# Kernel optimization log

Hardware: AMD Instinct MI355X
Metric: run time of the kernel (lower is better)

Reference implementation:

```python
import jax, jax.numpy as jnp
import numpy as np

BITS = 4
VALS_PER_WORD = 4  # four 4-bit nibbles packed per 16-bit word


def dequantize(w_packed, w_scale, w_bias, dtype):
    # w_packed: [out, groups, cols] int32, each word holds 4 nibbles (little-endian)
    out, g, cols = w_packed.shape
    shifts = jnp.arange(VALS_PER_WORD, dtype=jnp.int32) * BITS  # [4]
    # [out, groups, cols, 4] nibble values in [0, 15]
    q = (w_packed[..., None] >> shifts) & 0xF
    q = q.astype(dtype).reshape(out, g, cols * VALS_PER_WORD)
    w = q * w_scale + w_bias  # per-group affine dequant, scale/bias broadcast over group
    return w.reshape(out, g * cols * VALS_PER_WORD)  # [out, in]


def setup_inputs() -> dict:
    key = jax.random.key(0)
    k1, k2, k3, k4, k5 = jax.random.split(key, 5)
    B, S, IN, OUT, G = 2, 2048, 4096, 16384, 16
    cols = IN // G // VALS_PER_WORD  # 64 packed words per group
    return {
        "input": jax.random.normal(k1, (B, S, IN), dtype=jnp.float32),
        "w_packed": jax.random.randint(k2, (OUT, G, cols), 0, 65536, dtype=jnp.int32),
        "w_scale": jax.random.uniform(k3, (OUT, G, 1), dtype=jnp.float32) * 0.01,
        "w_bias": jax.random.normal(k4, (OUT, G, 1), dtype=jnp.float32) * 0.05,
        "bias": jax.random.normal(k5, (OUT,), dtype=jnp.float32),
    }


def reference(input, w_packed, w_scale, w_bias, bias):
    weight = dequantize(w_packed, w_scale, w_bias, input.dtype)  # [out, in]
    # F.linear: y = x @ W^T + b
    return jnp.einsum("bsi,oi->bso", input, weight) + bias
```

## Files before the change

### kernel.cpp

```cpp
#include <hip/hip_runtime.h>
#include <hip/hip_bf16.h>


typedef short bf16x8 __attribute__((ext_vector_type(8)));
typedef float f32x4 __attribute__((ext_vector_type(4)));
typedef int i32x4 __attribute__((ext_vector_type(4)));
typedef unsigned short u16;
typedef unsigned short u16x8 __attribute__((ext_vector_type(8)));

#define BM 128
#define BN 128
#define BK 64
#define THREADS 256

static __device__ __forceinline__ u16 f2bf(float f) {
    __hip_bfloat16 h = __float2bfloat16(f);
    return __builtin_bit_cast(u16, h);
}


__global__ void rowstat_kernel(const float* __restrict__ x, float* __restrict__ sx,
                               float* __restrict__ rsx, int K) {
    const int m = blockIdx.x;
    const int l = threadIdx.x;
    const float4* p = (const float4*)(x + (size_t)m * K);
    float mx = 0.f;
    for (int i = l; i < (K >> 2); i += 64) {
        const float4 v = p[i];
        mx = fmaxf(mx, fmaxf(fmaxf(fabsf(v.x), fabsf(v.y)),
                             fmaxf(fabsf(v.z), fabsf(v.w))));
    }
    #pragma unroll
    for (int o = 32; o; o >>= 1) mx = fmaxf(mx, __shfl_xor(mx, o));
    if (l == 0) {
        mx = fmaxf(mx, 1e-20f);
        sx[m]  = mx * (1.f / 127.f);
        rsx[m] = 127.f / mx;
    }
}

__global__ void quantX_kernel(const float* __restrict__ x, const float* __restrict__ rsx,
                              char* __restrict__ xq, int kshift, size_t n16) {
    size_t i = (size_t)blockIdx.x * blockDim.x + threadIdx.x;
    if (i >= n16) return;
    const int m = (int)((i * 16) >> kshift);
    const float r = rsx[m];
    const float4* px = (const float4*)(x + i * 16);
    int out[4];
    #pragma unroll
    for (int w = 0; w < 4; ++w) {
        const float4 v = px[w];
        const int b0 = __float2int_rn(v.x * r) & 0xFF;
        const int b1 = __float2int_rn(v.y * r) & 0xFF;
        const int b2 = __float2int_rn(v.z * r) & 0xFF;
        const int b3 = __float2int_rn(v.w * r) & 0xFF;
        out[w] = b0 | (b1 << 8) | (b2 << 16) | (b3 << 24);
    }
    *(int4*)(xq + i * 16) = make_int4(out[0], out[1], out[2], out[3]);
}

__global__ void rowscaleW_kernel(const float* __restrict__ Ws,
                                 const float* __restrict__ Wb,
                                 float* __restrict__ swr, float* __restrict__ rswr,
                                 int G, int N) {
    const int n = blockIdx.x * blockDim.x + threadIdx.x;
    if (n >= N) return;
    float mx = 1e-20f;
    for (int g = 0; g < G; ++g) {
        const float s = Ws[(size_t)n * G + g];
        const float b = Wb[(size_t)n * G + g];
        mx = fmaxf(mx, fmaxf(fabsf(b), fabsf(fmaf(15.f, s, b))));
    }
    swr[n]  = mx * (1.f / 127.f);
    rswr[n] = 127.f / mx;
}

__global__ void quantW_row_kernel(const int* __restrict__ Wp, const float* __restrict__ Ws,
                                  const float* __restrict__ Wb, const float* __restrict__ rswr,
                                  char* __restrict__ wq, int K, int G, int gshift,
                                  int kcshift, size_t nthr) {
    size_t t = (size_t)blockIdx.x * blockDim.x + threadIdx.x;
    if (t >= nthr) return;
    const int n  = (int)(t >> kcshift);
    const int kc = (int)(t & ((1u << kcshift) - 1));
    const int g  = (kc << 4) >> gshift;
    const float s = Ws[(size_t)n * G + g];
    const float b = Wb[(size_t)n * G + g];
    const float rs = rswr[n];
    const int4 wv = *(const int4*)(Wp + (size_t)n * (K >> 2) + ((size_t)kc << 2));
    const int wds[4] = {wv.x, wv.y, wv.z, wv.w};
    int out[4];
    #pragma unroll
    for (int w = 0; w < 4; ++w) {
        int o = 0;
        #pragma unroll
        for (int j = 0; j < 4; ++j) {
            const float v = fmaf((float)((wds[w] >> (4 * j)) & 0xF), s, b);
            o |= (__float2int_rn(v * rs) & 0xFF) << (8 * j);
        }
        out[w] = o;
    }
    *(int4*)(wq + t * 16) = make_int4(out[0], out[1], out[2], out[3]);
}


__global__ __launch_bounds__(256, 2)
void gql_gemm_i8t(const char* __restrict__ xq,
                  const char* __restrict__ wq,
                  const float* __restrict__ swr,
                  const float* __restrict__ sx,
                  const float* __restrict__ Bias,
                  float* __restrict__ Out,
                  int M, int N, int K)
{
    __shared__ __align__(16) char sA[2][256 * 64];
    __shared__ __align__(16) char sB[2][128 * 64];

    const int tid  = threadIdx.x;
    const int lane = tid & 63;
    const int wid  = tid >> 6;
    const int wm   = wid >> 1;
    const int wn   = wid & 1;

    const int nwg = gridDim.x;
    int wg = blockIdx.x;
    if ((nwg & 7) == 0) wg = (wg & 7) * (nwg >> 3) + (wg >> 3);
    const int nt = N / 128;
    const int m0 = (wg / nt) * 256;
    const int n0 = (wg % nt) * 128;

    const int fr = lane & 15;
    const int fq = lane >> 4;

    const int st_kc  = ((lane & 3) ^ ((lane >> 3) & 3)) << 4;
    const int st_rw  = lane >> 2;

    const int rq = (fq ^ ((fr >> 1) & 3)) << 4;

    i32x4 acc[8][4] = {};

    const int NT = K >> 6;

    auto stage = [&](int t, int buf) {
        const size_t k0 = (size_t)t << 6;
        #pragma unroll
        for (int i = 0; i < 4; ++i) {
            const int inst = wid + i * 4;
            const int row  = inst * 16 + st_rw;
            const char* src = xq + (size_t)(m0 + row) * K + k0 + st_kc;
            __builtin_amdgcn_global_load_lds(
                (const __attribute__((address_space(1))) void*)src,
                (__attribute__((address_space(3))) void*)&sA[buf][inst * 1024],
                16, 0, 0);
        }
        #pragma unroll
        for (int i = 0; i < 2; ++i) {
            const int inst = wid + i * 4;
            const int row  = inst * 16 + st_rw;
            const char* src = wq + (size_t)(n0 + row) * K + k0 + st_kc;
            __builtin_amdgcn_global_load_lds(
                (const __attribute__((address_space(1))) void*)src,
                (__attribute__((address_space(3))) void*)&sB[buf][inst * 1024],
                16, 0, 0);
        }
    };

    auto compute = [&](int buf) {
        i32x4 af[8], bfr[4];
        #pragma unroll
        for (int i = 0; i < 8; ++i) {
            const int row = wm * 128 + i * 16 + fr;
            const u16x8 raw = *(const u16x8*)(&sA[buf][row * 64 + rq]);
            af[i] = __builtin_bit_cast(i32x4, raw);
        }
        #pragma unroll
        for (int j = 0; j < 4; ++j) {
            const int row = wn * 64 + j * 16 + fr;
            const u16x8 raw = *(const u16x8*)(&sB[buf][row * 64 + rq]);
            bfr[j] = __builtin_bit_cast(i32x4, raw);
        }
        __builtin_amdgcn_s_setprio(1);
        #pragma unroll
        for (int i = 0; i < 8; ++i)
            #pragma unroll
            for (int j = 0; j < 4; ++j)
                acc[i][j] = __builtin_amdgcn_mfma_i32_16x16x64_i8(
                    af[i], bfr[j], acc[i][j], 0, 0, 0);
        __builtin_amdgcn_s_setprio(0);
    };

    stage(0, 0);
    int cur = 0;
    for (int t = 0; t < NT - 1; ++t) {
        stage(t + 1, cur ^ 1);
        __builtin_amdgcn_sched_barrier(0);
        asm volatile("s_waitcnt vmcnt(6)" ::: "memory");
        __builtin_amdgcn_s_barrier();
        asm volatile("" ::: "memory");
        compute(cur);
        __builtin_amdgcn_sched_barrier(0);
        asm volatile("" ::: "memory");
        __builtin_amdgcn_s_barrier();
        asm volatile("" ::: "memory");
        cur ^= 1;
    }
    asm volatile("s_waitcnt vmcnt(0)" ::: "memory");
    __builtin_amdgcn_s_barrier();
    asm volatile("" ::: "memory");
    compute(cur);

    #pragma unroll
    for (int j = 0; j < 4; ++j) {
        const int col = n0 + wn * 64 + j * 16 + fr;
        const float bv = Bias[col];
        const float sv = swr[col];
        #pragma unroll
        for (int i = 0; i < 8; ++i) {
            const int mb = m0 + wm * 128 + i * 16 + (fq << 2);
            #pragma unroll
            for (int r = 0; r < 4; ++r)
                Out[(size_t)(mb + r) * N + col] =
                    fmaf(sx[mb + r] * sv, (float)acc[i][j][r], bv);
        }
    }
}


__global__ void cvtA_kernel(const float* __restrict__ A, u16* __restrict__ wsA,
                            size_t n8) {
    size_t i = (size_t)blockIdx.x * blockDim.x + threadIdx.x;
    if (i >= n8) return;
    const float4 v0 = *(const float4*)(A + i * 8);
    const float4 v1 = *(const float4*)(A + i * 8 + 4);
    u16x8 h;
    h[0] = f2bf(v0.x); h[1] = f2bf(v0.y); h[2] = f2bf(v0.z); h[3] = f2bf(v0.w);
    h[4] = f2bf(v1.x); h[5] = f2bf(v1.y); h[6] = f2bf(v1.z); h[7] = f2bf(v1.w);
    *(u16x8*)(wsA + i * 8) = h;
}

__global__ void deqW_kernel(const int* __restrict__ Wp, const float* __restrict__ Ws,
                            const float* __restrict__ Wb, u16* __restrict__ wsW,
                            int K, int G, int gshift, int kgshift, size_t n8) {
    size_t t = (size_t)blockIdx.x * blockDim.x + threadIdx.x;
    if (t >= n8) return;
    const int n  = (int)(t >> kgshift);
    const int kg = (int)(t & ((1u << kgshift) - 1));
    const int k  = kg << 3;
    const int g  = k >> gshift;
    const float s = Ws[n * G + g];
    const float b = Wb[n * G + g];
    const int2 w2 = *(const int2*)(Wp + (size_t)n * (K >> 2) + (k >> 2));
    u16x8 h;
    #pragma unroll
    for (int j = 0; j < 4; ++j)
        h[j]     = f2bf(fmaf((float)((w2.x >> (4 * j)) & 0xF), s, b));
    #pragma unroll
    for (int j = 0; j < 4; ++j)
        h[4 + j] = f2bf(fmaf((float)((w2.y >> (4 * j)) & 0xF), s, b));
    *(u16x8*)(wsW + ((size_t)n << (kgshift + 3)) + k) = h;
}

__global__ __launch_bounds__(THREADS, 2)
void gql_gemm_pre(const u16* __restrict__ wsA,
                  const u16* __restrict__ wsW,
                  const float* __restrict__ Bias,
                  float* __restrict__ Out,
                  int M, int N, int K)
{
    __shared__ __align__(16) u16 sA[BM * BK];
    __shared__ __align__(16) u16 sB[BN * BK];

    const int tid  = threadIdx.x;
    const int lane = tid & 63;
    const int wid  = tid >> 6;

    const int nwg = gridDim.x;
    int wg = blockIdx.x;
    if ((nwg & 7) == 0) wg = (wg & 7) * (nwg >> 3) + (wg >> 3);
    const int nt     = N / BN;
    const int m0 = (wg / nt) * BM;
    const int n0 = (wg % nt) * BN;

    const int st_r  = (lane >> 3);
    const int st_g  = lane & 7;

    const int wr = (wid >> 1) << 6;
    const int wc = (wid & 1) << 6;
    const int fr = lane & 15;
    const int fq = lane >> 4;

    f32x4 acc[4][4] = {};

    for (int k0 = 0; k0 < K; k0 += BK) {
        __syncthreads();

        #pragma unroll
        for (int i = 0; i < 4; ++i) {
            const int r = wid * 32 + i * 8 + st_r;
            const int gsrc = (st_g ^ (r & 7)) << 3;
            const u16* srcA = wsA + (size_t)(m0 + r) * K + k0 + gsrc;
            const u16* srcB = wsW + (size_t)(n0 + r) * K + k0 + gsrc;
            __builtin_amdgcn_global_load_lds(
                (const __attribute__((address_space(1))) void*)srcA,
                (__attribute__((address_space(3))) void*)&sA[(wid * 32 + i * 8) * BK],
                16, 0, 0);
            __builtin_amdgcn_global_load_lds(
                (const __attribute__((address_space(1))) void*)srcB,
                (__attribute__((address_space(3))) void*)&sB[(wid * 32 + i * 8) * BK],
                16, 0, 0);
        }

        __syncthreads();

        #pragma unroll
        for (int sub = 0; sub < 2; ++sub) {
            const int kch = (sub << 2) + fq;
            bf16x8 af[4], bfg[4];
            #pragma unroll
            for (int i = 0; i < 4; ++i) {
                const int row = wr + i * 16 + fr;
                af[i] = *(const bf16x8*)((const char*)sA + row * (BK * 2)
                                         + (((kch ^ (row & 7)) << 4)));
            }
            #pragma unroll
            for (int j = 0; j < 4; ++j) {
                const int row = wc + j * 16 + fr;
                bfg[j] = *(const bf16x8*)((const char*)sB + row * (BK * 2)
                                          + (((kch ^ (row & 7)) << 4)));
            }
            #pragma unroll
            for (int i = 0; i < 4; ++i)
                #pragma unroll
                for (int j = 0; j < 4; ++j)
                    acc[i][j] = __builtin_amdgcn_mfma_f32_16x16x32_bf16(
                        af[i], bfg[j], acc[i][j], 0, 0, 0);
        }
    }

    #pragma unroll
    for (int j = 0; j < 4; ++j) {
        const int n = n0 + wc + j * 16 + fr;
        const float bvv = Bias[n];
        #pragma unroll
        for (int i = 0; i < 4; ++i) {
            const int mb = m0 + wr + i * 16 + (fq << 2);
            #pragma unroll
            for (int r = 0; r < 4; ++r)
                Out[(size_t)(mb + r) * N + n] = acc[i][j][r] + bvv;
        }
    }
}


__global__ __launch_bounds__(THREADS, 2)
void gql_gemm(const float* __restrict__ A,
              const int* __restrict__ Wp,
              const float* __restrict__ Ws,
              const float* __restrict__ Wb,
              const float* __restrict__ Bias,
              float* __restrict__ Out,
              int M, int N, int K, int G, int gshift)
{
    __shared__ __align__(16) u16 sA[BM * BK];
    __shared__ __align__(16) u16 sB[BN * BK];

    const int tid  = threadIdx.x;
    const int lane = tid & 63;
    const int wid  = tid >> 6;

    const int nwg = gridDim.x;
    int wg = blockIdx.x;
    if ((nwg & 7) == 0) wg = (wg & 7) * (nwg >> 3) + (wg >> 3);
    const int nt     = N / BN;
    const int m0 = (wg / nt) * BM;
    const int n0 = (wg % nt) * BN;

    const int wpr = K >> 2;

    const int a_r = tid >> 4;
    const int a_c = (tid & 15) << 2;
    const int b_r = tid >> 3;
    const int b_w = (tid & 7) << 1;

    const int wr = (wid >> 1) << 6;
    const int wc = (wid & 1) << 6;
    const int fr = lane & 15;
    const int fq = lane >> 4;

    f32x4 acc[4][4] = {};

    for (int k0 = 0; k0 < K; k0 += BK) {
        __syncthreads();

        #pragma unroll
        for (int it = 0; it < 8; ++it) {
            const int row = it * 16 + a_r;
            const float4 v = *(const float4*)(A + (size_t)(m0 + row) * K + (k0 + a_c));
            u16 h0 = f2bf(v.x), h1 = f2bf(v.y), h2 = f2bf(v.z), h3 = f2bf(v.w);
            const int byte = (a_c << 1) ^ ((row & 7) << 4);
            *(u16*)((char*)sA + row * (BK * 2) + byte + 0) = h0;
            *(u16*)((char*)sA + row * (BK * 2) + byte + 2) = h1;
            *(u16*)((char*)sA + row * (BK * 2) + byte + 4) = h2;
            *(u16*)((char*)sA + row * (BK * 2) + byte + 6) = h3;
        }

        const int g = k0 >> gshift;
        #pragma unroll
        for (int it = 0; it < 4; ++it) {
            const int row = it * 32 + b_r;
            const int gn  = n0 + row;
            const int2 w2 = *(const int2*)(Wp + (size_t)gn * wpr + (k0 >> 2) + b_w);
            const float s = Ws[gn * G + g];
            const float b = Wb[gn * G + g];
            u16x8 h;
            #pragma unroll
            for (int j = 0; j < 4; ++j)
                h[j]     = f2bf(fmaf((float)((w2.x >> (4 * j)) & 0xF), s, b));
            #pragma unroll
            for (int j = 0; j < 4; ++j)
                h[4 + j] = f2bf(fmaf((float)((w2.y >> (4 * j)) & 0xF), s, b));
            const int byte = (b_w << 3) ^ ((row & 7) << 4);
            *(u16x8*)((char*)sB + row * (BK * 2) + byte) = h;
        }

        __syncthreads();

        #pragma unroll
        for (int sub = 0; sub < 2; ++sub) {
            const int kch = (sub << 2) + fq;
            bf16x8 af[4], bfg[4];
            #pragma unroll
            for (int i = 0; i < 4; ++i) {
                const int row = wr + i * 16 + fr;
                af[i] = *(const bf16x8*)((const char*)sA + row * (BK * 2)
                                         + ((kch << 4) ^ ((row & 7) << 4)));
            }
            #pragma unroll
            for (int j = 0; j < 4; ++j) {
                const int row = wc + j * 16 + fr;
                bfg[j] = *(const bf16x8*)((const char*)sB + row * (BK * 2)
                                          + ((kch << 4) ^ ((row & 7) << 4)));
            }
            #pragma unroll
            for (int i = 0; i < 4; ++i)
                #pragma unroll
                for (int j = 0; j < 4; ++j)
                    acc[i][j] = __builtin_amdgcn_mfma_f32_16x16x32_bf16(
                        af[i], bfg[j], acc[i][j], 0, 0, 0);
        }
    }

    #pragma unroll
    for (int j = 0; j < 4; ++j) {
        const int n = n0 + wc + j * 16 + fr;
        const float bvv = Bias[n];
        #pragma unroll
        for (int i = 0; i < 4; ++i) {
            const int mb = m0 + wr + i * 16 + (fq << 2);
            #pragma unroll
            for (int r = 0; r < 4; ++r)
                Out[(size_t)(mb + r) * N + n] = acc[i][j][r] + bvv;
        }
    }
}

extern "C" void kernel_launch(void* const* d_in, const int* in_sizes, int n_in,
                              void* d_out, int out_size, void* d_ws, size_t ws_size,
                              hipStream_t stream) {
    const float* A    = (const float*)d_in[0];
    const int*   Wp   = (const int*)d_in[1];
    const float* Ws   = (const float*)d_in[2];
    const float* Wb   = (const float*)d_in[3];
    const float* Bias = (const float*)d_in[4];
    float* Out = (float*)d_out;

    const int OUT  = in_sizes[4];
    const int OG   = in_sizes[2];
    const int G    = OG / OUT;
    const int cols = in_sizes[1] / OG;
    const int IN   = G * cols * 4;
    const int M    = in_sizes[0] / IN;

    const int gk = IN / G;
    int gshift = 0;
    while ((1 << gshift) < gk) ++gshift;

    int kshift = 0;
    while ((1 << kshift) < IN) ++kshift;

    const size_t needXq = (size_t)M * IN;
    const size_t needWq = (size_t)OUT * IN;
    const size_t needSc = (size_t)M * 8 + (size_t)OUT * 8;
    const size_t needI8 = needXq + needWq + needSc;

    const bool kpow2  = ((IN & (IN - 1)) == 0);
    const bool gkpow2 = ((1 << gshift) == gk);

    if (ws_size >= needI8 && kpow2 && gkpow2 && (IN % 256) == 0 &&
        (M % 256) == 0 && (OUT % 128) == 0 && (gk % 16) == 0) {
        char*  xq   = (char*)d_ws;
        char*  wq   = (char*)d_ws + needXq;
        float* sx   = (float*)((char*)d_ws + needXq + needWq);
        float* rsx  = sx + M;
        float* swr  = rsx + M;
        float* rswr = swr + OUT;

        rowstat_kernel<<<M, 64, 0, stream>>>(A, sx, rsx, IN);

        const size_t n16 = (size_t)M * IN / 16;
        quantX_kernel<<<(unsigned)((n16 + 255) / 256), 256, 0, stream>>>(
            A, rsx, xq, kshift, n16);

        rowscaleW_kernel<<<(OUT + 255) / 256, 256, 0, stream>>>(Ws, Wb, swr, rswr,
                                                                G, OUT);

        const int kcshift = kshift - 4;
        const size_t nthr = (size_t)OUT * (IN >> 4);
        quantW_row_kernel<<<(unsigned)((nthr + 255) / 256), 256, 0, stream>>>(
            Wp, Ws, Wb, rswr, wq, IN, G, gshift, kcshift, nthr);

        dim3 grid((M / 256) * (OUT / 128));
        gql_gemm_i8t<<<grid, 256, 0, stream>>>(xq, wq, swr, sx, Bias, Out,
                                               M, OUT, IN);
        return;
    }

    const size_t needA = (size_t)M * IN * 2;
    const size_t needW = (size_t)OUT * IN * 2;

    if (ws_size >= needA + needW && (IN & 7) == 0 &&
        (M % 128) == 0 && (OUT % 128) == 0 && (IN % 64) == 0) {
        u16* wsA = (u16*)d_ws;
        u16* wsW = (u16*)((char*)d_ws + needA);

        const size_t nA8 = (size_t)M * IN / 8;
        cvtA_kernel<<<(unsigned)((nA8 + 255) / 256), 256, 0, stream>>>(A, wsA, nA8);

        int kgshift = 0;
        while ((1 << kgshift) < (IN >> 3)) ++kgshift;
        const size_t nW8 = (size_t)OUT * IN / 8;
        deqW_kernel<<<(unsigned)((nW8 + 255) / 256), 256, 0, stream>>>(
            Wp, Ws, Wb, wsW, IN, G, gshift, kgshift, nW8);

        dim3 grid((M / BM) * (OUT / BN));
        gql_gemm_pre<<<grid, THREADS, 0, stream>>>(wsA, wsW, Bias, Out, M, OUT, IN);
    } else {
        dim3 grid((M / BM) * (OUT / BN));
        gql_gemm<<<grid, THREADS, 0, stream>>>(A, Wp, Ws, Wb, Bias, Out,
                                               M, OUT, IN, G, gshift);
    }
}
```

Measured before the change: 388.4 us.

## Enlarge int8 GEMM tile to 256x256 with 8 waves and 4-stage LDS pipeline

The int8 MFMA GEMM moves from a 256x128 tile with 4 waves to a 256x256 tile with 8 waves (512 threads), which halves the grid. Double buffering becomes a 4-slot ring that prefetches three K-tiles ahead, so the loop needs only one barrier per iteration instead of two. The aim is more data reuse per block and a deeper overlap of global-to-LDS loads with MFMA work. The cost is about 128KB of LDS per block, which allows only one block per CU, and OUT must now be a multiple of 256.

```diff
diff --git a/kernel.cpp b/kernel.cpp
--- a/kernel.cpp
+++ b/kernel.cpp
@@ -104,8 +104,8 @@
 }
 
 
-__global__ __launch_bounds__(256, 2)
-void gql_gemm_i8t(const char* __restrict__ xq,
+__global__ __launch_bounds__(512, 2)
+void gql_gemm_i8q(const char* __restrict__ xq,
                   const char* __restrict__ wq,
                   const float* __restrict__ swr,
                   const float* __restrict__ sx,
@@ -113,70 +113,69 @@
                   float* __restrict__ Out,
                   int M, int N, int K)
 {
-    __shared__ __align__(16) char sA[2][256 * 64];
-    __shared__ __align__(16) char sB[2][128 * 64];
+    __shared__ __align__(16) char sA[4][256 * 64];
+    __shared__ __align__(16) char sB[4][256 * 64];
 
     const int tid  = threadIdx.x;
     const int lane = tid & 63;
     const int wid  = tid >> 6;
-    const int wm   = wid >> 1;
-    const int wn   = wid & 1;
+    const int wm   = wid >> 2;
+    const int wn   = wid & 3;
 
     const int nwg = gridDim.x;
     int wg = blockIdx.x;
     if ((nwg & 7) == 0) wg = (wg & 7) * (nwg >> 3) + (wg >> 3);
-    const int nt = N / 128;
+    const int nt = N / 256;
     const int m0 = (wg / nt) * 256;
-    const int n0 = (wg % nt) * 128;
+    const int n0 = (wg % nt) * 256;
 
     const int fr = lane & 15;
     const int fq = lane >> 4;
 
-    const int st_kc  = ((lane & 3) ^ ((lane >> 3) & 3)) << 4;
-    const int st_rw  = lane >> 2;
-
+    const int st_kc = ((lane & 3) ^ ((lane >> 3) & 3)) << 4;
+    const int st_rw = lane >> 2;
     const int rq = (fq ^ ((fr >> 1) & 3)) << 4;
 
     i32x4 acc[8][4] = {};
 
     const int NT = K >> 6;
 
-    auto stage = [&](int t, int buf) {
+    auto stage = [&](int t, int slot) {
         const size_t k0 = (size_t)t << 6;
         #pragma unroll
-        for (int i = 0; i < 4; ++i) {
-            const int inst = wid + i * 4;
+        for (int i = 0; i < 2; ++i) {
+            const int inst = wid + i * 8;
             const int row  = inst * 16 + st_rw;
             const char* src = xq + (size_t)(m0 + row) * K + k0 + st_kc;
             __builtin_amdgcn_global_load_lds(
                 (const __attribute__((address_space(1))) void*)src,
-                (__attribute__((address_space(3))) void*)&sA[buf][inst * 1024],
+                (__attribute__((address_space(3))) void*)&sA[slot][inst * 1024],
                 16, 0, 0);
         }
         #pragma unroll
         for (int i = 0; i < 2; ++i) {
-            const int inst = wid + i * 4;
+            const int inst = wid + i * 8;
             const int row  = inst * 16 + st_rw;
             const char* src = wq + (size_t)(n0 + row) * K + k0 + st_kc;
             __builtin_amdgcn_global_load_lds(
                 (const __attribute__((address_space(1))) void*)src,
-                (__attribute__((address_space(3))) void*)&sB[buf][inst * 1024],
+                (__attribute__((address_space(3))) void*)&sB[slot][inst * 1024],
                 16, 0, 0);
         }
     };
 
-    auto compute = [&](int buf) {
+    auto compute = [&](int slot) {
         i32x4 af[8], bfr[4];
         #pragma unroll
         for (int i = 0; i < 8; ++i) {
             const int row = wm * 128 + i * 16 + fr;
-            const u16x8 raw = *(const u16x8*)(&sA[buf][row * 64 + rq]);
+            const u16x8 raw = *(const u16x8*)(&sA[slot][row * 64 + rq]);
             af[i] = __builtin_bit_cast(i32x4, raw);
         }
         #pragma unroll
         for (int j = 0; j < 4; ++j) {
             const int row = wn * 64 + j * 16 + fr;
-            const u16x8 raw = *(const u16x8*)(&sB[buf][row * 64 + rq]);
+            const u16x8 raw = *(const u16x8*)(&sB[slot][row * 64 + rq]);
             bfr[j] = __builtin_bit_cast(i32x4, raw);
         }
         __builtin_amdgcn_s_setprio(1);
@@ -189,25 +188,19 @@
         __builtin_amdgcn_s_setprio(0);
     };
 
-    stage(0, 0);
-    int cur = 0;
-    for (int t = 0; t < NT - 1; ++t) {
-        stage(t + 1, cur ^ 1);
+    stage(0, 0); stage(1, 1); stage(2, 2);
+
+    for (int t = 0; t < NT; ++t) {
+        asm volatile("s_waitcnt vmcnt(8)" ::: "memory");
         __builtin_amdgcn_sched_barrier(0);
-        asm volatile("s_waitcnt vmcnt(6)" ::: "memory");
         __builtin_amdgcn_s_barrier();
         asm volatile("" ::: "memory");
-        compute(cur);
-        __builtin_amdgcn_sched_barrier(0);
-        asm volatile("" ::: "memory");
-        __builtin_amdgcn_s_barrier();
-        asm volatile("" ::: "memory");
-        cur ^= 1;
-    }
+        const int tn = (t + 3 < NT) ? (t + 3) : (NT - 1);
+        stage(tn, (t + 3) & 3);
+        compute(t & 3);
+    }
+
     asm volatile("s_waitcnt vmcnt(0)" ::: "memory");
-    __builtin_amdgcn_s_barrier();
-    asm volatile("" ::: "memory");
-    compute(cur);
 
     #pragma unroll
     for (int j = 0; j < 4; ++j) {
@@ -497,7 +490,7 @@
     const bool gkpow2 = ((1 << gshift) == gk);
 
     if (ws_size >= needI8 && kpow2 && gkpow2 && (IN % 256) == 0 &&
-        (M % 256) == 0 && (OUT % 128) == 0 && (gk % 16) == 0) {
+        (M % 256) == 0 && (OUT % 256) == 0 && (gk % 16) == 0) {
         char*  xq   = (char*)d_ws;
         char*  wq   = (char*)d_ws + needXq;
         float* sx   = (float*)((char*)d_ws + needXq + needWq);
@@ -519,8 +512,8 @@
         quantW_row_kernel<<<(unsigned)((nthr + 255) / 256), 256, 0, stream>>>(
             Wp, Ws, Wb, rswr, wq, IN, G, gshift, kcshift, nthr);
 
-        dim3 grid((M / 256) * (OUT / 128));
-        gql_gemm_i8t<<<grid, 256, 0, stream>>>(xq, wq, swr, sx, Bias, Out,
+        dim3 grid((M / 256) * (OUT / 256));
+        gql_gemm_i8q<<<grid, 512, 0, stream>>>(xq, wq, swr, sx, Bias, Out,
                                                M, OUT, IN);
         return;
     }
```

After: 414.3 us. 1.07x slower.
